# Optimization experiments

Measured on AMD Instinct MI355X. Metric: run time of the kernel, lower is better.

## Reference

```python
import jax, jax.numpy as jnp
import numpy as np

EMBED_DIM = 1024
HIDDEN = 128
N_QUERY = 65536
N_PROTO = 512


def setup_inputs() -> dict:
    key = jax.random.key(0)
    k1, k2, k3, k4, k5, k6, k7 = jax.random.split(key, 7)
    d2 = EMBED_DIM * 2
    lim1 = 1.0 / np.sqrt(d2)
    lim2 = 1.0 / np.sqrt(HIDDEN)
    return {
        "query_features": jax.random.normal(k1, (N_QUERY, EMBED_DIM), dtype=jnp.float32),
        "prototypes": jax.random.normal(k2, (N_PROTO, EMBED_DIM), dtype=jnp.float32),
        "distances": jax.random.uniform(k3, (N_QUERY, N_PROTO), dtype=jnp.float32),
        "W1": jax.random.uniform(k4, (d2, HIDDEN), minval=-lim1, maxval=lim1, dtype=jnp.float32),
        "b1": jax.random.uniform(k5, (HIDDEN,), minval=-lim1, maxval=lim1, dtype=jnp.float32),
        "W2": jax.random.uniform(k6, (HIDDEN, 1), minval=-lim2, maxval=lim2, dtype=jnp.float32),
        "b2": jax.random.uniform(k7, (1,), minval=-lim2, maxval=lim2, dtype=jnp.float32),
    }


def reference(query_features, prototypes, distances, W1, b1, W2, b2):
    # Batched version of the per-query loop: argmin -> gather -> concat -> MLP.
    idx = jnp.argmin(distances, axis=1)                      # [N_QUERY]
    closest = prototypes[idx]                                # [N_QUERY, D]
    combined = jnp.concatenate([query_features, closest], axis=-1)  # [N_QUERY, 2D]
    h = jax.nn.relu(combined @ W1 + b1)                      # [N_QUERY, 128]
    out = jax.nn.sigmoid(h @ W2 + b2)                        # [N_QUERY, 1]
    return jnp.squeeze(out, axis=-1)                         # [N_QUERY]
```

## Files before the change

kernel.cpp:

```cpp
#include <hip/hip_runtime.h>
#include <math.h>

#define EMBED 1024
#define HIDDEN 128
#define NPROTO 512

typedef short bf16x8 __attribute__((ext_vector_type(8)));
typedef float f32x4 __attribute__((ext_vector_type(4)));
typedef unsigned int u32x4 __attribute__((ext_vector_type(4)));

__device__ __forceinline__ unsigned short f2bf(float x) {
    unsigned u = __builtin_bit_cast(unsigned, x);
    return (unsigned short)((u + 0x8000u) >> 16);
}
__device__ __forceinline__ unsigned pk2(float a, float b) {
    unsigned ua = __builtin_bit_cast(unsigned, a) + 0x8000u;
    unsigned ub = __builtin_bit_cast(unsigned, b) + 0x8000u;
    return (ua >> 16) | (ub & 0xFFFF0000u);
}

#define GLL16(gptr, lptr)                                                \
    __builtin_amdgcn_global_load_lds(                                    \
        (const __attribute__((address_space(1))) void*)(gptr),           \
        (__attribute__((address_space(3))) void*)(lptr), 16, 0, 0)

__global__ __launch_bounds__(256) void prep_kernel(
    const float* __restrict__ prototypes,
    const float* __restrict__ W1,
    float* __restrict__ proto_h,
    unsigned short* __restrict__ w1t)
{
    int b = blockIdx.x;
    int t = threadIdx.x;
    if (b < 512) {
        __shared__ float s_part[128];
        int ks = t >> 7, h = t & 127;
        const float* pr = prototypes + (size_t)b * EMBED + ks * 512;
        const float* w  = W1 + (size_t)(EMBED + ks * 512) * HIDDEN + h;
        float acc = 0.f;
        for (int k = 0; k < 512; k += 8) {
            #pragma unroll
            for (int j = 0; j < 8; ++j)
                acc += pr[k + j] * w[(size_t)(k + j) * HIDDEN];
        }
        if (ks) s_part[h] = acc;
        __syncthreads();
        if (!ks) proto_h[(size_t)b * HIDDEN + h] = acc + s_part[h];
    } else {
        int s = (b - 512) * 256 + t;
        int n = s & 127;
        int k0 = (s >> 7) * 8;
        bf16x8 v;
        #pragma unroll
        for (int j = 0; j < 8; ++j)
            v[j] = (short)f2bf(W1[(size_t)(k0 + j) * HIDDEN + n]);
        *(bf16x8*)(w1t + (size_t)n * EMBED + k0) = v;
    }
}

__global__ __launch_bounds__(256, 2) void main_kernel(
    const float* __restrict__ qf,
    const float* __restrict__ dist,
    const float* __restrict__ b1,
    const float* __restrict__ W2,
    const float* __restrict__ b2,
    const float* __restrict__ proto_h,
    const unsigned short* __restrict__ w1t,
    float* __restrict__ out)
{
    __shared__ __align__(16) char lds_a[3][16384];
    __shared__ __align__(16) char lds_b[3][8192];
    __shared__ int s_idx[4][32];

    const int t = threadIdx.x;
    const int wave = t >> 6, lane = t & 63;
    const int quad = lane >> 4, tid16 = lane & 15;
    const int q0  = blockIdx.x * 128;
    const int q0w = q0 + wave * 32;

    const char* gA[4];
    {
        int rsub = lane >> 1;
        int hlog = (lane & 1) ^ ((lane >> 3) & 1);
        #pragma unroll
        for (int i = 0; i < 4; ++i) {
            int row = i * 32 + rsub;
            gA[i] = (const char*)(qf + (size_t)(q0 + row) * EMBED + wave * 8 + hlog * 4);
        }
    }
    const char* gB[2];
    #pragma unroll
    for (int i = 0; i < 2; ++i)
        gB[i] = (const char*)(w1t + (size_t)(i * 64 + lane) * EMBED + wave * 8);

#define STAGE(buf) do {                                                  \
        char* la_ = &lds_a[buf][(wave * 4) * 1024];                      \
        char* lb_ = &lds_b[buf][(wave * 2) * 1024];                      \
        _Pragma("unroll")                                                \
        for (int i_ = 0; i_ < 4; ++i_) {                                 \
            GLL16(gA[i_], la_ + i_ * 1024); gA[i_] += 128;               \
        }                                                                \
        _Pragma("unroll")                                                \
        for (int i_ = 0; i_ < 2; ++i_) {                                 \
            GLL16(gB[i_], lb_ + i_ * 1024); gB[i_] += 64;                \
        }                                                                \
    } while (0)

    STAGE(0);
    STAGE(1);

#define AMLD(st, base) do {                                              \
        _Pragma("unroll")                                                \
        for (int j_ = 0; j_ < 4; ++j_) {                                 \
            const float* dr_ = dist + (size_t)(q0w + (base) + j_) * NPROTO; \
            st[2 * j_]     = ((const float4*)dr_)[lane];                 \
            st[2 * j_ + 1] = ((const float4*)dr_)[lane + 64];            \
        }                                                                \
    } while (0)
#define AMPROC(st, base) do {                                            \
        _Pragma("unroll")                                                \
        for (int j_ = 0; j_ < 4; ++j_) {                                 \
            float4 v0 = st[2 * j_], v1 = st[2 * j_ + 1];                 \
            float bv = v0.x; int bi = lane * 4;                          \
            if (v0.y < bv) { bv = v0.y; bi = lane * 4 + 1; }             \
            if (v0.z < bv) { bv = v0.z; bi = lane * 4 + 2; }             \
            if (v0.w < bv) { bv = v0.w; bi = lane * 4 + 3; }             \
            int c_ = 256 + lane * 4;                                     \
            if (v1.x < bv) { bv = v1.x; bi = c_; }                       \
            if (v1.y < bv) { bv = v1.y; bi = c_ + 1; }                   \
            if (v1.z < bv) { bv = v1.z; bi = c_ + 2; }                   \
            if (v1.w < bv) { bv = v1.w; bi = c_ + 3; }                   \
            _Pragma("unroll")                                            \
            for (int s_ = 1; s_ < 64; s_ <<= 1) {                        \
                float ov = __shfl_xor(bv, s_);                           \
                int   oi = __shfl_xor(bi, s_);                           \
                if (ov < bv || (ov == bv && oi < bi)) { bv = ov; bi = oi; } \
            }                                                            \
            if (lane == 0) s_idx[wave][(base) + j_] = bi;                \
        }                                                                \
    } while (0)

    {
        float4 A0[8], A1[8], A2[8];
        AMLD(A0, 0);  AMLD(A1, 4);
        AMLD(A2, 8);  AMPROC(A0, 0);
        AMLD(A0, 12); AMPROC(A1, 4);
        AMLD(A1, 16); AMPROC(A2, 8);
        AMLD(A2, 20); AMPROC(A0, 12);
        AMLD(A0, 24); AMPROC(A1, 16);
        AMLD(A1, 28); AMPROC(A2, 20);
        AMPROC(A0, 24);
        AMPROC(A1, 28);
    }

    f32x4 acc[2][8];
    #pragma unroll
    for (int mi = 0; mi < 2; ++mi)
        #pragma unroll
        for (int ni = 0; ni < 8; ++ni)
            acc[mi][ni] = (f32x4){0.f, 0.f, 0.f, 0.f};

    const int aoff = quad * 4096 + (wave * 32 + tid16) * 32 + ((tid16 >> 2) & 1) * 16;
    const int boff = quad * 2048 + tid16 * 16;

#define COMPUTE(buf) do {                                                \
        bf16x8 bfr[8];                                                   \
        _Pragma("unroll")                                                \
        for (int ni_ = 0; ni_ < 8; ++ni_)                                \
            bfr[ni_] = *(const bf16x8*)(&lds_b[buf][boff + ni_ * 256]);  \
        _Pragma("unroll")                                                \
        for (int mi_ = 0; mi_ < 2; ++mi_) {                              \
            float4 lo = *(const float4*)(&lds_a[buf][aoff + mi_ * 512]); \
            float4 hi = *(const float4*)(&lds_a[buf][(aoff ^ 16) + mi_ * 512]); \
            u32x4 p_;                                                    \
            p_.x = pk2(lo.x, lo.y); p_.y = pk2(lo.z, lo.w);              \
            p_.z = pk2(hi.x, hi.y); p_.w = pk2(hi.z, hi.w);              \
            bf16x8 af = __builtin_bit_cast(bf16x8, p_);                  \
            _Pragma("unroll")                                            \
            for (int ni_ = 0; ni_ < 8; ++ni_)                            \
                acc[mi_][ni_] = __builtin_amdgcn_mfma_f32_16x16x32_bf16( \
                    af, bfr[ni_], acc[mi_][ni_], 0, 0, 0);               \
        }                                                                \
    } while (0)

    int bufr = 0, bufs = 2;
    for (int kt = 0; kt < 31; ++kt) {
        asm volatile("s_waitcnt vmcnt(6)\n\ts_barrier" ::: "memory");
        if (kt < 30) {
            STAGE(bufs);
            bufs = (bufs == 2) ? 0 : bufs + 1;
        }
        COMPUTE(bufr);
        bufr = (bufr == 2) ? 0 : bufr + 1;
    }
    asm volatile("s_waitcnt vmcnt(0)\n\ts_barrier" ::: "memory");
    COMPUTE(bufr);

    float b1v[8], w2v[8];
    #pragma unroll
    for (int ni = 0; ni < 8; ++ni) {
        b1v[ni] = b1[ni * 16 + tid16];
        w2v[ni] = W2[ni * 16 + tid16];
    }
    const float b2v = b2[0];
    #pragma unroll
    for (int mi = 0; mi < 2; ++mi) {
        #pragma unroll
        for (int r = 0; r < 4; ++r) {
            int m = mi * 16 + quad * 4 + r;
            const float* ph = proto_h + (size_t)s_idx[wave][m] * HIDDEN + tid16;
            float sum = 0.f;
            #pragma unroll
            for (int ni = 0; ni < 8; ++ni) {
                float v = acc[mi][ni][r] + b1v[ni] + ph[ni * 16];
                sum += fmaxf(v, 0.f) * w2v[ni];
            }
            #pragma unroll
            for (int s = 1; s < 16; s <<= 1) sum += __shfl_xor(sum, s);
            if (tid16 == 0) out[q0w + m] = 1.f / (1.f + expf(-(sum + b2v)));
        }
    }
#undef STAGE
#undef AMLD
#undef AMPROC
#undef COMPUTE
}

extern "C" void kernel_launch(void* const* d_in, const int* in_sizes, int n_in,
                              void* d_out, int out_size, void* d_ws, size_t ws_size,
                              hipStream_t stream) {
    const float* qf    = (const float*)d_in[0];
    const float* proto = (const float*)d_in[1];
    const float* dist  = (const float*)d_in[2];
    const float* W1    = (const float*)d_in[3];
    const float* b1    = (const float*)d_in[4];
    const float* W2    = (const float*)d_in[5];
    const float* b2    = (const float*)d_in[6];
    float* out = (float*)d_out;

    float* proto_h = (float*)d_ws;
    unsigned short* w1t = (unsigned short*)((char*)d_ws + 512 * 128 * 4);

    prep_kernel<<<576, 256, 0, stream>>>(proto, W1, proto_h, w1t);

    int nq = in_sizes[0] / EMBED;
    main_kernel<<<nq / 128, 256, 0, stream>>>(qf, dist, b1, W2, b2, proto_h, w1t, out);
}
```

Measured before the change: 486.7 us.

## Load query tiles straight to registers and stage W1 in larger swizzled LDS chunks

Query rows no longer pass through LDS. Each wave loads its own A fragments from global memory into registers, software-pipelined two k-steps ahead, and converts them to bf16 there. W1 is staged as 32 KB swizzled chunks in a double-buffered LDS layout, so there are 8 barriers instead of 32. The argmin prologue is also simplified into plain batches. This removes LDS traffic and barrier overhead for A, but relies on register-direct global loads keeping enough bytes in flight and raises register pressure.

After: 484.6 us. About the same (-0.4%).

```diff
diff --git a/kernel.cpp b/kernel.cpp
--- a/kernel.cpp
+++ b/kernel.cpp
@@ -68,8 +68,7 @@
     const unsigned short* __restrict__ w1t,
     float* __restrict__ out)
 {
-    __shared__ __align__(16) char lds_a[3][16384];
-    __shared__ __align__(16) char lds_b[3][8192];
+    __shared__ __align__(16) char lds_b[2][32768];
     __shared__ int s_idx[4][32];
 
     const int t = threadIdx.x;
@@ -78,79 +77,74 @@
     const int q0  = blockIdx.x * 128;
     const int q0w = q0 + wave * 32;
 
-    const char* gA[4];
-    {
-        int rsub = lane >> 1;
-        int hlog = (lane & 1) ^ ((lane >> 3) & 1);
-        #pragma unroll
-        for (int i = 0; i < 4; ++i) {
-            int row = i * 32 + rsub;
-            gA[i] = (const char*)(qf + (size_t)(q0 + row) * EMBED + wave * 8 + hlog * 4);
-        }
-    }
-    const char* gB[2];
-    #pragma unroll
-    for (int i = 0; i < 2; ++i)
-        gB[i] = (const char*)(w1t + (size_t)(i * 64 + lane) * EMBED + wave * 8);
-
-#define STAGE(buf) do {                                                  \
-        char* la_ = &lds_a[buf][(wave * 4) * 1024];                      \
-        char* lb_ = &lds_b[buf][(wave * 2) * 1024];                      \
-        _Pragma("unroll")                                                \
-        for (int i_ = 0; i_ < 4; ++i_) {                                 \
-            GLL16(gA[i_], la_ + i_ * 1024); gA[i_] += 128;               \
+    const int ln = lane >> 4, lk = (lane & 15) * 16;
+    const size_t off_e = (size_t)ln * 2048 + (lk ^ (ln << 4));
+    const size_t off_o = (size_t)ln * 2048 + (lk ^ (((4 + ln) & 7) << 4));
+    const char* wsrc = (const char*)w1t + (size_t)wave * 65536;
+
+#define STAGE_B(c, buf) do {                                             \
+        char* lb_ = &lds_b[buf][wave * 8192];                            \
+        _Pragma("unroll")                                                \
+        for (int g_ = 0; g_ < 8; ++g_)                                   \
+            GLL16(wsrc + g_ * 8192 + (c) * 256 + ((g_ & 1) ? off_o : off_e), \
+                  lb_ + g_ * 1024);                                      \
+    } while (0)
+
+    const float* abase = qf + (size_t)(q0w + tid16) * EMBED + quad * 8;
+
+#define LOADA(dst, s) do {                                               \
+        _Pragma("unroll")                                                \
+        for (int mi_ = 0; mi_ < 2; ++mi_) {                              \
+            const float* p_ = abase + (size_t)(mi_ * 16) * EMBED + (s) * 32; \
+            dst[mi_][0] = ((const float4*)p_)[0];                        \
+            dst[mi_][1] = ((const float4*)p_)[1];                        \
         }                                                                \
-        _Pragma("unroll")                                                \
-        for (int i_ = 0; i_ < 2; ++i_) {                                 \
-            GLL16(gB[i_], lb_ + i_ * 1024); gB[i_] += 64;                \
+    } while (0)
+
+#define CVT(af, src) do {                                                \
+        _Pragma("unroll")                                                \
+        for (int mi_ = 0; mi_ < 2; ++mi_) {                              \
+            u32x4 p_;                                                    \
+            p_.x = pk2(src[mi_][0].x, src[mi_][0].y);                    \
+            p_.y = pk2(src[mi_][0].z, src[mi_][0].w);                    \
+            p_.z = pk2(src[mi_][1].x, src[mi_][1].y);                    \
+            p_.w = pk2(src[mi_][1].z, src[mi_][1].w);                    \
+            af[mi_] = __builtin_bit_cast(bf16x8, p_);                    \
         }                                                                \
     } while (0)
 
-    STAGE(0);
-    STAGE(1);
-
-#define AMLD(st, base) do {                                              \
-        _Pragma("unroll")                                                \
-        for (int j_ = 0; j_ < 4; ++j_) {                                 \
-            const float* dr_ = dist + (size_t)(q0w + (base) + j_) * NPROTO; \
-            st[2 * j_]     = ((const float4*)dr_)[lane];                 \
-            st[2 * j_ + 1] = ((const float4*)dr_)[lane + 64];            \
-        }                                                                \
-    } while (0)
-#define AMPROC(st, base) do {                                            \
-        _Pragma("unroll")                                                \
-        for (int j_ = 0; j_ < 4; ++j_) {                                 \
-            float4 v0 = st[2 * j_], v1 = st[2 * j_ + 1];                 \
-            float bv = v0.x; int bi = lane * 4;                          \
-            if (v0.y < bv) { bv = v0.y; bi = lane * 4 + 1; }             \
-            if (v0.z < bv) { bv = v0.z; bi = lane * 4 + 2; }             \
-            if (v0.w < bv) { bv = v0.w; bi = lane * 4 + 3; }             \
-            int c_ = 256 + lane * 4;                                     \
-            if (v1.x < bv) { bv = v1.x; bi = c_; }                       \
-            if (v1.y < bv) { bv = v1.y; bi = c_ + 1; }                   \
-            if (v1.z < bv) { bv = v1.z; bi = c_ + 2; }                   \
-            if (v1.w < bv) { bv = v1.w; bi = c_ + 3; }                   \
-            _Pragma("unroll")                                            \
-            for (int s_ = 1; s_ < 64; s_ <<= 1) {                        \
-                float ov = __shfl_xor(bv, s_);                           \
-                int   oi = __shfl_xor(bi, s_);                           \
-                if (ov < bv || (ov == bv && oi < bi)) { bv = ov; bi = oi; } \
-            }                                                            \
-            if (lane == 0) s_idx[wave][(base) + j_] = bi;                \
-        }                                                                \
-    } while (0)
-
-    {
-        float4 A0[8], A1[8], A2[8];
-        AMLD(A0, 0);  AMLD(A1, 4);
-        AMLD(A2, 8);  AMPROC(A0, 0);
-        AMLD(A0, 12); AMPROC(A1, 4);
-        AMLD(A1, 16); AMPROC(A2, 8);
-        AMLD(A2, 20); AMPROC(A0, 12);
-        AMLD(A0, 24); AMPROC(A1, 16);
-        AMLD(A1, 28); AMPROC(A2, 20);
-        AMPROC(A0, 24);
-        AMPROC(A1, 28);
+    STAGE_B(0, 0);
+    float4 a0[2][2], a1[2][2];
+    LOADA(a0, 0);
+    LOADA(a1, 1);
+
+    for (int i = 0; i < 32; i += 4) {
+        float4 v0[4], v1[4];
+        #pragma unroll
+        for (int j = 0; j < 4; ++j) {
+            const float* dr = dist + (size_t)(q0w + i + j) * NPROTO;
+            v0[j] = ((const float4*)dr)[lane];
+            v1[j] = ((const float4*)dr)[lane + 64];
+        }
+        #pragma unroll
+        for (int j = 0; j < 4; ++j) {
+            float bv = v0[j].x; int bi = lane * 4;
+            if (v0[j].y < bv) { bv = v0[j].y; bi = lane * 4 + 1; }
+            if (v0[j].z < bv) { bv = v0[j].z; bi = lane * 4 + 2; }
+            if (v0[j].w < bv) { bv = v0[j].w; bi = lane * 4 + 3; }
+            int c = 256 + lane * 4;
+            if (v1[j].x < bv) { bv = v1[j].x; bi = c; }
+            if (v1[j].y < bv) { bv = v1[j].y; bi = c + 1; }
+            if (v1[j].z < bv) { bv = v1[j].z; bi = c + 2; }
+            if (v1[j].w < bv) { bv = v1[j].w; bi = c + 3; }
+            #pragma unroll
+            for (int s = 1; s < 64; s <<= 1) {
+                float ov = __shfl_xor(bv, s);
+                int   oi = __shfl_xor(bi, s);
+                if (ov < bv || (ov == bv && oi < bi)) { bv = ov; bi = oi; }
+            }
+            if (lane == 0) s_idx[wave][i + j] = bi;
+        }
     }
 
     f32x4 acc[2][8];
@@ -160,41 +154,36 @@
         for (int ni = 0; ni < 8; ++ni)
             acc[mi][ni] = (f32x4){0.f, 0.f, 0.f, 0.f};
 
-    const int aoff = quad * 4096 + (wave * 32 + tid16) * 32 + ((tid16 >> 2) & 1) * 16;
-    const int boff = quad * 2048 + tid16 * 16;
-
-#define COMPUTE(buf) do {                                                \
+    const int Lb = tid16 * 256 + ((quad ^ (tid16 & 3)) << 4)
+                 + (((tid16 >> 2) & 1) << 6);
+
+#define STEP(s, buf) do {                                                \
+        bf16x8 af[2];                                                    \
+        if ((s) & 1) { CVT(af, a1); if ((s) + 2 < 32) LOADA(a1, (s) + 2); } \
+        else         { CVT(af, a0); if ((s) + 2 < 32) LOADA(a0, (s) + 2); } \
+        const char* pb = &lds_b[buf][(Lb ^ (((s) & 1) << 6))             \
+                                     + (((s) >> 1) & 1) * 128];          \
         bf16x8 bfr[8];                                                   \
         _Pragma("unroll")                                                \
         for (int ni_ = 0; ni_ < 8; ++ni_)                                \
-            bfr[ni_] = *(const bf16x8*)(&lds_b[buf][boff + ni_ * 256]);  \
-        _Pragma("unroll")                                                \
-        for (int mi_ = 0; mi_ < 2; ++mi_) {                              \
-            float4 lo = *(const float4*)(&lds_a[buf][aoff + mi_ * 512]); \
-            float4 hi = *(const float4*)(&lds_a[buf][(aoff ^ 16) + mi_ * 512]); \
-            u32x4 p_;                                                    \
-            p_.x = pk2(lo.x, lo.y); p_.y = pk2(lo.z, lo.w);              \
-            p_.z = pk2(hi.x, hi.y); p_.w = pk2(hi.z, hi.w);              \
-            bf16x8 af = __builtin_bit_cast(bf16x8, p_);                  \
+            bfr[ni_] = *(const bf16x8*)(pb + ni_ * 4096);                \
+        _Pragma("unroll")                                                \
+        for (int mi_ = 0; mi_ < 2; ++mi_)                                \
             _Pragma("unroll")                                            \
             for (int ni_ = 0; ni_ < 8; ++ni_)                            \
                 acc[mi_][ni_] = __builtin_amdgcn_mfma_f32_16x16x32_bf16( \
-                    af, bfr[ni_], acc[mi_][ni_], 0, 0, 0);               \
-        }                                                                \
-    } while (0)
-
-    int bufr = 0, bufs = 2;
-    for (int kt = 0; kt < 31; ++kt) {
-        asm volatile("s_waitcnt vmcnt(6)\n\ts_barrier" ::: "memory");
-        if (kt < 30) {
-            STAGE(bufs);
-            bufs = (bufs == 2) ? 0 : bufs + 1;
-        }
-        COMPUTE(bufr);
-        bufr = (bufr == 2) ? 0 : bufr + 1;
-    }
-    asm volatile("s_waitcnt vmcnt(0)\n\ts_barrier" ::: "memory");
-    COMPUTE(bufr);
+                    af[mi_], bfr[ni_], acc[mi_][ni_], 0, 0, 0);          \
+    } while (0)
+
+    #pragma unroll
+    for (int c = 0; c < 8; ++c) {
+        __syncthreads();
+        if (c < 7) STAGE_B(c + 1, (c + 1) & 1);
+        STEP(c * 4 + 0, c & 1);
+        STEP(c * 4 + 1, c & 1);
+        STEP(c * 4 + 2, c & 1);
+        STEP(c * 4 + 3, c & 1);
+    }
 
     float b1v[8], w2v[8];
     #pragma unroll
@@ -220,10 +209,10 @@
             if (tid16 == 0) out[q0w + m] = 1.f / (1.f + expf(-(sum + b2v)));
         }
     }
-#undef STAGE
-#undef AMLD
-#undef AMPROC
-#undef COMPUTE
+#undef STAGE_B
+#undef LOADA
+#undef CVT
+#undef STEP
 }
 
 extern "C" void kernel_launch(void* const* d_in, const int* in_sizes, int n_in,
```
